# Kernel tuning notes

Hardware: AMD Instinct MI355X
Metric: run time of the kernel (lower is better)

The kernel has to match this reference:

```python
import jax, jax.numpy as jnp
import numpy as np

EMBED_DIM = 768
NUM_HEADS = 12
SEGMENT_LENGTHS = (2048, 4096, 8192)
DILATION_RATES = (1, 2, 4)
LN_EPS = 1e-5


def setup_inputs() -> dict:
    key = jax.random.key(0)
    ks = jax.random.split(key, 12)
    B, N, E = 2, 8192, EMBED_DIM
    xavier = (2.0 / (E + E)) ** 0.5  # xavier_normal_ std for square weight
    return {
        "query": jax.random.normal(ks[0], (B, N, E), jnp.float32),
        "key_": jax.random.normal(ks[1], (B, N, E), jnp.float32),
        "value": jax.random.normal(ks[2], (B, N, E), jnp.float32),
        "Wq": jax.random.normal(ks[3], (E, E), jnp.float32) * xavier,
        "bq": jnp.zeros((E,), jnp.float32),
        "Wk": jax.random.normal(ks[4], (E, E), jnp.float32) * xavier,
        "bk": jnp.zeros((E,), jnp.float32),
        "Wv": jax.random.normal(ks[5], (E, E), jnp.float32) * xavier,
        "bv": jnp.zeros((E,), jnp.float32),
        "Wo": jax.random.normal(ks[6], (E, E), jnp.float32) * xavier,
        "bo": jnp.zeros((E,), jnp.float32),
        "ln_g": jnp.ones((E,), jnp.float32),
        "ln_b": jnp.zeros((E,), jnp.float32),
    }


def _dilated_attention(q, k, v):
    # q,k,v: [b, n, h, d]  (LongNet dilated attention, non-causal)
    b, n, h, d = q.shape
    G = len(SEGMENT_LENGTHS)
    hpg = h // G  # heads per dilation group
    scale = 1.0 / jnp.sqrt(jnp.asarray(d, q.dtype))
    out = jnp.zeros_like(q)
    for i, (g, r) in enumerate(zip(SEGMENT_LENGTHS, DILATION_RATES)):
        offset = i % r
        hmin, hmax = i * hpg, (i + 1) * hpg
        def seg(x):
            # [b, n_seg, g, h, d] -> dilate within segment, slice head group
            xs = x.reshape(b, n // g, g, h, d)
            return xs[:, :, offset::r, hmin:hmax, :]  # [b, ns, s, hg, d]
        qs, ks_, vs = seg(q), seg(k), seg(v)
        # attention within each dilated segment
        scores = jnp.einsum("bnshd,bnthd->bnhst", qs, ks_) * scale
        attn = jax.nn.softmax(scores, axis=-1)
        xo = jnp.einsum("bnhst,bnthd->bnshd", attn, vs)
        out_r = out.reshape(b, n // g, g, h, d)
        out_r = out_r.at[:, :, offset::r, hmin:hmax, :].add(xo)
        out = out_r.reshape(b, n, h, d)
    return out / G


def reference(query, key_, value, Wq, bq, Wk, bk, Wv, bv, Wo, bo, ln_g, ln_b):
    b, n, e = query.shape
    h, d = NUM_HEADS, e // NUM_HEADS
    q = (query @ Wq.T + bq).reshape(b, n, h, d)
    k = (key_ @ Wk.T + bk).reshape(b, n, h, d)
    v = (value @ Wv.T + bv).reshape(b, n, h, d)
    x = _dilated_attention(q, k, v).reshape(b, n, e)
    mu = jnp.mean(x, axis=-1, keepdims=True)
    var = jnp.mean(jnp.square(x - mu), axis=-1, keepdims=True)
    x = (x - mu) * jax.lax.rsqrt(var + LN_EPS) * ln_g + ln_b
    return x @ Wo.T + bo
```

## Files before the change

kernel.cpp:

```cpp
#include <hip/hip_runtime.h>
#include <hip/hip_bf16.h>
#include <stdint.h>

typedef unsigned int uint32;
typedef unsigned short u16;
typedef __attribute__((ext_vector_type(4))) float f32x4;
typedef __attribute__((ext_vector_type(16))) float f32x16;
typedef __attribute__((ext_vector_type(8))) __bf16 bf16x8;
typedef __attribute__((ext_vector_type(8))) short i16x8;
typedef __attribute__((ext_vector_type(4))) short i16x4;
typedef __attribute__((ext_vector_type(4))) uint32 u32x4;

#define DEVINL static __device__ __forceinline__

DEVINL u16 f2bf(float f){
  uint32 u = __builtin_bit_cast(uint32, f);
  return (u16)((u + 0x7fffu + ((u >> 16) & 1u)) >> 16);
}

DEVINL uint32 cvtpk(float lo, float hi){
  uint32 r;
  asm("v_cvt_pk_bf16_f32 %0, %1, %2" : "=v"(r) : "v"(lo), "v"(hi));
  return r;
}

DEVINL void permswap(uint32 &a, uint32 &b){
  asm volatile("s_nop 1\n\tv_permlane32_swap_b32 %0, %1" : "+v"(a), "+v"(b));
}

DEVINL f32x4 mfma16(bf16x8 a, bf16x8 b, f32x4 c){
  return __builtin_amdgcn_mfma_f32_16x16x32_bf16(a, b, c, 0, 0, 0);
}
DEVINL f32x16 mfma32(bf16x8 a, bf16x8 b, f32x16 c){
  return __builtin_amdgcn_mfma_f32_32x32x16_bf16(a, b, c, 0, 0, 0);
}
DEVINL f32x16 zero16(){
  f32x16 z;
  #pragma unroll
  for (int r = 0; r < 16; ++r) z[r] = 0.f;
  return z;
}

DEVINL void gload16(const u16* g, u16* l){
  __builtin_amdgcn_global_load_lds(
      (const __attribute__((address_space(1))) uint32*)g,
      (__attribute__((address_space(3))) uint32*)l, 16, 0, 0);
}

static constexpr size_t ISTR = 2048 * 64;
static constexpr float QSCALE = 0.18033688011112042f;
static constexpr int LDA = 40;

__global__ void cvt_w4(const float* __restrict__ s0, const float* __restrict__ s1,
                       const float* __restrict__ s2, const float* __restrict__ s3,
                       u16* __restrict__ d0, u16* __restrict__ d1,
                       u16* __restrict__ d2, u16* __restrict__ d3, int n4){
  const int wsel = blockIdx.y;
  const float* src = wsel == 0 ? s0 : wsel == 1 ? s1 : wsel == 2 ? s2 : s3;
  u16* dst = wsel == 0 ? d0 : wsel == 1 ? d1 : wsel == 2 ? d2 : d3;
  int i = blockIdx.x * 256 + threadIdx.x;
  if (i < n4){
    f32x4 v = *(const f32x4*)(src + (size_t)i * 4);
    u16 o[4];
    #pragma unroll
    for (int j = 0; j < 4; ++j) o[j] = f2bf(v[j]);
    *(i16x4*)(dst + (size_t)i * 4) = *(const i16x4*)o;
  }
}

__global__ __launch_bounds__(256) void qkv_fused(
    const float* __restrict__ X0, const float* __restrict__ X1, const float* __restrict__ X2,
    const u16* __restrict__ W0, const u16* __restrict__ W1, const u16* __restrict__ W2,
    const float* __restrict__ b0, const float* __restrict__ b1, const float* __restrict__ b2,
    u16* __restrict__ Y0, u16* __restrict__ Y1, u16* __restrict__ Y2)
{
  __shared__ u16 As[2][128 * LDA];
  __shared__ u16 Bs[2][128 * 32];
  const int tid = threadIdx.x;
  const int l = tid & 63, w = tid >> 6;
  const int l15 = l & 15, lh = l >> 4;
  const int wr = w >> 1, wc = w & 1;
  const int yb = blockIdx.y;
  const int sect = yb / 6;
  const int row0 = blockIdx.x * 128, col0 = (yb % 6) * 128;

  const float* X   = sect == 0 ? X0 : sect == 1 ? X1 : X2;
  const u16*   W   = sect == 0 ? W0 : sect == 1 ? W1 : W2;
  const float* bia_p = sect == 0 ? b0 : sect == 1 ? b1 : b2;
  u16*         Yg  = sect == 0 ? Y0 : sect == 1 ? Y1 : Y2;
  const float scale = sect == 0 ? QSCALE : 1.0f;
  const int tmode = (sect == 2) ? 1 : 0;

  const int gr = l >> 2;
  const int gcx = ((l & 3) ^ ((gr >> 1) & 3)) * 8;
  const u16* wsrc0 = W + (size_t)(col0 + w * 32 + gr) * 768 + gcx;

  const int sr = tid >> 1, sc = (tid & 1) * 16;
  const float* asrc = X + (size_t)(row0 + sr) * 768 + sc;

  f32x4 acc[4][4];
  #pragma unroll
  for (int i = 0; i < 4; ++i)
    #pragma unroll
    for (int j = 0; j < 4; ++j) acc[i][j] = f32x4{0.f, 0.f, 0.f, 0.f};

  auto STAGE_B = [&](int buf, int ks){
    const u16* ws = wsrc0 + ks * 32;
    gload16(ws,            &Bs[buf][(w * 32) * 32]);
    gload16(ws + 16 * 768, &Bs[buf][(w * 32 + 16) * 32]);
  };
  auto WRITE_A = [&](int buf, f32x4 ra0, f32x4 ra1, f32x4 ra2, f32x4 ra3){
    u32x4 w0 = { cvtpk(ra0[0], ra0[1]), cvtpk(ra0[2], ra0[3]),
                 cvtpk(ra1[0], ra1[1]), cvtpk(ra1[2], ra1[3]) };
    u32x4 w1 = { cvtpk(ra2[0], ra2[1]), cvtpk(ra2[2], ra2[3]),
                 cvtpk(ra3[0], ra3[1]), cvtpk(ra3[2], ra3[3]) };
    *(i16x8*)&As[buf][sr * LDA + sc]     = __builtin_bit_cast(i16x8, w0);
    *(i16x8*)&As[buf][sr * LDA + sc + 8] = __builtin_bit_cast(i16x8, w1);
  };

  {
    STAGE_B(0, 0);
    f32x4 ra0 = *(const f32x4*)(asrc);
    f32x4 ra1 = *(const f32x4*)(asrc + 4);
    f32x4 ra2 = *(const f32x4*)(asrc + 8);
    f32x4 ra3 = *(const f32x4*)(asrc + 12);
    WRITE_A(0, ra0, ra1, ra2, ra3);
  }
  asm volatile("s_waitcnt vmcnt(0)");
  __syncthreads();

  const int bxor = ((l15 >> 1) & 3) * 8;
  int cur = 0;
  for (int ks = 0; ks < 24; ++ks) {
    const int nxt = cur ^ 1;
    f32x4 ra0, ra1, ra2, ra3;
    const bool has = ks < 23;
    if (has) {
      STAGE_B(nxt, ks + 1);
      const float* ap = asrc + (ks + 1) * 32;
      ra0 = *(const f32x4*)(ap);      ra1 = *(const f32x4*)(ap + 4);
      ra2 = *(const f32x4*)(ap + 8);  ra3 = *(const f32x4*)(ap + 12);
    }
    bf16x8 af[4], bfr[4];
    #pragma unroll
    for (int mi = 0; mi < 4; ++mi)
      af[mi] = *(const bf16x8*)&As[cur][(wr * 64 + mi * 16 + l15) * LDA + lh * 8];
    #pragma unroll
    for (int ni = 0; ni < 4; ++ni)
      bfr[ni] = *(const bf16x8*)&Bs[cur][(wc * 64 + ni * 16 + l15) * 32 + ((lh * 8) ^ bxor)];
    #pragma unroll
    for (int mi = 0; mi < 4; ++mi)
      #pragma unroll
      for (int ni = 0; ni < 4; ++ni)
        acc[mi][ni] = mfma16(af[mi], bfr[ni], acc[mi][ni]);
    if (has) WRITE_A(nxt, ra0, ra1, ra2, ra3);
    asm volatile("s_waitcnt vmcnt(0)");
    __syncthreads();
    cur = nxt;
  }

  #pragma unroll
  for (int ni = 0; ni < 4; ++ni) {
    const int e = col0 + wc * 64 + ni * 16 + l15;
    const int h = e >> 6, d = e & 63;
    const int grp = h >> 2, hg = h & 3;
    const int instB = (grp == 0) ? 0 : (grp == 1) ? 32 : 48;
    const float bia = bia_p[e];
    #pragma unroll
    for (int mi = 0; mi < 4; ++mi) {
      #pragma unroll
      for (int r = 0; r < 4; ++r) {
        const int row = row0 + wr * 64 + mi * 16 + lh * 4 + r;
        const int b = row >> 13, nn = row & 8191;
        const int p = nn & ((2048 << grp) - 1);
        if ((p & ((1 << grp) - 1)) != grp) continue;
        const int seg = nn >> (11 + grp);
        const int t = (p - grp) >> grp;
        const int inst = instB + ((b * (4 >> grp) + seg) << 2) + hg;
        const u16 val = f2bf((acc[mi][ni][r] + bia) * scale);
        if (tmode == 0) Yg[(size_t)inst * ISTR + (size_t)t * 64 + d] = val;
        else            Yg[(size_t)inst * ISTR + (size_t)d * 2048 + t] = val;
      }
    }
  }
}

__global__ __launch_bounds__(256) void dil_attn(
    const u16* __restrict__ Qg, const u16* __restrict__ Kg,
    const u16* __restrict__ VgT, uint32* __restrict__ Op32, float* __restrict__ Ls)
{
  __shared__ u16 Kb[2][64 * 64];
  __shared__ u16 Vb[2][64 * 64];
  const int tid = threadIdx.x;
  const int w = tid >> 6, l = tid & 63;
  const int l31 = l & 31, hi = l >> 5;
  const int id = blockIdx.x;
  const int nid = (id & 7) * 224 + (id >> 3);
  const int inst = nid >> 5, rem = nid & 31;
  const int qb = rem >> 1, kh = rem & 1;
  const size_t ibase = (size_t)inst * ISTR;
  const int qbase = qb * 128 + w * 32;
  const int k0base = kh * 1024;

  const u16* qlane = Qg + ibase + (size_t)(qbase + l31) * 64 + hi * 8;
  const bf16x8 qf0 = *(const bf16x8*)(qlane);
  const bf16x8 qf1 = *(const bf16x8*)(qlane + 16);
  const bf16x8 qf2 = *(const bf16x8*)(qlane + 32);
  const bf16x8 qf3 = *(const bf16x8*)(qlane + 48);

  const int srow = l >> 3;
  const int scol = ((l & 7) ^ (srow & 7)) << 3;
  const u16* kgs = Kg  + ibase + (size_t)srow * 64 + scol;
  const u16* vgs = VgT + ibase + (size_t)srow * 2048 + scol;

  f32x16 acc0 = zero16(), acc1 = zero16(), rs = zero16();
  const int sxor = (l31 & 7) << 3;
  const bf16x8 ones = __builtin_bit_cast(bf16x8,
      u32x4{0x3F803F80u, 0x3F803F80u, 0x3F803F80u, 0x3F803F80u});

  auto STAGE = [&](int buf, int k0){
    #pragma unroll
    for (int q = 0; q < 2; ++q){
      const int rb = w * 16 + q * 8;
      gload16(kgs + (size_t)(k0 + rb) * 64, &Kb[buf][rb * 64]);
      gload16(vgs + (size_t)rb * 2048 + k0, &Vb[buf][rb * 64]);
    }
  };

  STAGE(0, k0base);
  asm volatile("s_waitcnt vmcnt(0)");
  __syncthreads();

  int cur = 0;
  for (int step = 0; step < 16; ++step) {
    if (step < 15) STAGE(cur ^ 1, k0base + ((step + 1) << 6));
    const u16* kt = &Kb[cur][0];
    const u16* vt = &Vb[cur][0];
    #pragma unroll
    for (int s = 0; s < 2; ++s) {
      const int ksub = s * 32;
      const int krow = (ksub + l31) * 64;
      bf16x8 kc0 = *(const bf16x8*)&kt[krow + ((hi * 8)      ^ sxor)];
      bf16x8 kc1 = *(const bf16x8*)&kt[krow + ((16 + hi * 8) ^ sxor)];
      bf16x8 kc2 = *(const bf16x8*)&kt[krow + ((32 + hi * 8) ^ sxor)];
      bf16x8 kc3 = *(const bf16x8*)&kt[krow + ((48 + hi * 8) ^ sxor)];

      f32x16 sT = zero16();
      sT = mfma32(kc0, qf0, sT);
      sT = mfma32(kc1, qf1, sT);
      sT = mfma32(kc2, qf2, sT);
      sT = mfma32(kc3, qf3, sT);

      #pragma unroll
      for (int r = 0; r < 16; ++r) sT[r] = __builtin_amdgcn_exp2f(sT[r]);

      uint32 cw0 = cvtpk(sT[0],  sT[1]),  cw1 = cvtpk(sT[2],  sT[3]);
      uint32 cw2 = cvtpk(sT[4],  sT[5]),  cw3 = cvtpk(sT[6],  sT[7]);
      uint32 cw4 = cvtpk(sT[8],  sT[9]),  cw5 = cvtpk(sT[10], sT[11]);
      uint32 cw6 = cvtpk(sT[12], sT[13]), cw7 = cvtpk(sT[14], sT[15]);
      permswap(cw0, cw2); permswap(cw1, cw3);
      permswap(cw4, cw6); permswap(cw5, cw7);
      bf16x8 pa0 = __builtin_bit_cast(bf16x8, u32x4{cw0, cw1, cw2, cw3});
      bf16x8 pa1 = __builtin_bit_cast(bf16x8, u32x4{cw4, cw5, cw6, cw7});

      const int vr0 = l31 * 64, vr1 = (l31 + 32) * 64;
      bf16x8 v00 = *(const bf16x8*)&vt[vr0 + ((ksub + hi * 8)      ^ sxor)];
      bf16x8 v01 = *(const bf16x8*)&vt[vr0 + ((ksub + 16 + hi * 8) ^ sxor)];
      bf16x8 v10 = *(const bf16x8*)&vt[vr1 + ((ksub + hi * 8)      ^ sxor)];
      bf16x8 v11 = *(const bf16x8*)&vt[vr1 + ((ksub + 16 + hi * 8) ^ sxor)];

      rs   = mfma32(pa0, ones, rs);
      rs   = mfma32(pa1, ones, rs);
      acc0 = mfma32(pa0, v00, acc0);
      acc0 = mfma32(pa1, v01, acc0);
      acc1 = mfma32(pa0, v10, acc1);
      acc1 = mfma32(pa1, v11, acc1);
    }
    asm volatile("s_waitcnt vmcnt(0)");
    __syncthreads();
    cur ^= 1;
  }

  if (l31 == 0) {
    float* lsp = Ls + ((size_t)kh * 56 + inst) * 2048 + qbase;
    #pragma unroll
    for (int r = 0; r < 16; ++r) {
      const int qrow = (r & 3) + 8 * (r >> 2) + 4 * hi;
      lsp[qrow] = rs[r];
    }
  }
  uint32* op = Op32 + (size_t)kh * (56u * 2048u * 32u)
                    + ((size_t)inst * 2048 + qbase) * 32 + l31;
  #pragma unroll
  for (int r = 0; r < 16; ++r) {
    const int qrow = (r & 3) + 8 * (r >> 2) + 4 * hi;
    op[(size_t)qrow * 32] = cvtpk(acc0[r], acc1[r]);
  }
}

__global__ __launch_bounds__(256) void ln_gather(
    const uint32* __restrict__ Op32, const float* __restrict__ Ls,
    const float* __restrict__ gamma, const float* __restrict__ beta,
    u16* __restrict__ xln)
{
  const int row = blockIdx.x;
  const int b = row >> 13, nn = row & 8191;
  const int tid = threadIdx.x;
  const size_t KHOFF = 56u * 2048u * 32u;
  float v[3];
  #pragma unroll
  for (int j = 0; j < 3; ++j) {
    const int e = tid + j * 256;
    const int h = e >> 6, d = e & 63;
    const int grp = h >> 2, hg = h & 3;
    const int p = nn & ((2048 << grp) - 1);
    float val = 0.f;
    if ((p & ((1 << grp) - 1)) == grp) {
      const int seg = nn >> (11 + grp);
      const int instB = (grp == 0) ? 0 : (grp == 1) ? 32 : 48;
      const int inst = instB + ((b * (4 >> grp) + seg) << 2) + hg;
      const int t = (p - grp) >> grp;
      const size_t wbase = ((size_t)inst * 2048 + t) * 32 + (d & 31);
      const uint32 w0 = Op32[wbase];
      const uint32 w1 = Op32[wbase + KHOFF];
      const float o0 = __builtin_bit_cast(float, d < 32 ? (w0 << 16) : (w0 & 0xFFFF0000u));
      const float o1 = __builtin_bit_cast(float, d < 32 ? (w1 << 16) : (w1 & 0xFFFF0000u));
      const float s = Ls[(size_t)inst * 2048 + t] + Ls[(size_t)(56 * 2048) + inst * 2048 + t];
      val = (o0 + o1) * (1.0f / (3.0f * s));
    }
    v[j] = val;
  }
  float s = v[0] + v[1] + v[2];
  float q = v[0]*v[0] + v[1]*v[1] + v[2]*v[2];
  #pragma unroll
  for (int off = 1; off < 64; off <<= 1) { s += __shfl_xor(s, off); q += __shfl_xor(q, off); }
  __shared__ float red[8];
  const int w = tid >> 6, l = tid & 63;
  if (l == 0) { red[w] = s; red[4 + w] = q; }
  __syncthreads();
  s = red[0] + red[1] + red[2] + red[3];
  q = red[4] + red[5] + red[6] + red[7];
  const float mu = s * (1.f / 768.f);
  const float var = q * (1.f / 768.f) - mu * mu;
  const float rs = rsqrtf(var + 1e-5f);
  #pragma unroll
  for (int j = 0; j < 3; ++j) {
    const int e = tid + j * 256;
    xln[(size_t)row * 768 + e] = f2bf((v[j] - mu) * rs * gamma[e] + beta[e]);
  }
}

__global__ __launch_bounds__(256) void out_gemm(
    const u16* __restrict__ Xb, const u16* __restrict__ W,
    const float* __restrict__ bias, float* __restrict__ out)
{
  __shared__ u16 As[2][128 * 32];
  __shared__ u16 Bs[2][128 * 32];
  const int tid = threadIdx.x;
  const int l = tid & 63, w = tid >> 6;
  const int l15 = l & 15, lh = l >> 4;
  const int wr = w >> 1, wc = w & 1;
  const int row0 = blockIdx.x * 128, col0 = blockIdx.y * 128;

  const int gr = l >> 2;
  const int gcx = ((l & 3) ^ ((gr >> 1) & 3)) * 8;
  const u16* asrc0 = Xb + (size_t)(row0 + w * 32 + gr) * 768 + gcx;
  const u16* wsrc0 = W  + (size_t)(col0 + w * 32 + gr) * 768 + gcx;

  f32x4 acc[4][4];
  #pragma unroll
  for (int i = 0; i < 4; ++i)
    #pragma unroll
    for (int j = 0; j < 4; ++j) acc[i][j] = f32x4{0.f, 0.f, 0.f, 0.f};

  auto STAGE = [&](int buf, int ks){
    const u16* as = asrc0 + ks * 32;
    const u16* ws = wsrc0 + ks * 32;
    gload16(as,            &As[buf][(w * 32) * 32]);
    gload16(as + 16 * 768, &As[buf][(w * 32 + 16) * 32]);
    gload16(ws,            &Bs[buf][(w * 32) * 32]);
    gload16(ws + 16 * 768, &Bs[buf][(w * 32 + 16) * 32]);
  };

  STAGE(0, 0);
  asm volatile("s_waitcnt vmcnt(0)");
  __syncthreads();

  const int bxor = ((l15 >> 1) & 3) * 8;
  int cur = 0;
  for (int ks = 0; ks < 24; ++ks) {
    const int nxt = cur ^ 1;
    if (ks < 23) STAGE(nxt, ks + 1);
    bf16x8 af[4], bfr[4];
    #pragma unroll
    for (int mi = 0; mi < 4; ++mi)
      af[mi] = *(const bf16x8*)&As[cur][(wr * 64 + mi * 16 + l15) * 32 + ((lh * 8) ^ bxor)];
    #pragma unroll
    for (int ni = 0; ni < 4; ++ni)
      bfr[ni] = *(const bf16x8*)&Bs[cur][(wc * 64 + ni * 16 + l15) * 32 + ((lh * 8) ^ bxor)];
    #pragma unroll
    for (int mi = 0; mi < 4; ++mi)
      #pragma unroll
      for (int ni = 0; ni < 4; ++ni)
        acc[mi][ni] = mfma16(af[mi], bfr[ni], acc[mi][ni]);
    asm volatile("s_waitcnt vmcnt(0)");
    __syncthreads();
    cur = nxt;
  }

  #pragma unroll
  for (int ni = 0; ni < 4; ++ni) {
    const int e = col0 + wc * 64 + ni * 16 + l15;
    const float bia = bias[e];
    #pragma unroll
    for (int mi = 0; mi < 4; ++mi) {
      #pragma unroll
      for (int r = 0; r < 4; ++r) {
        const int row = row0 + wr * 64 + mi * 16 + lh * 4 + r;
        out[(size_t)row * 768 + e] = acc[mi][ni][r] + bia;
      }
    }
  }
}

extern "C" void kernel_launch(void* const* d_in, const int* in_sizes, int n_in,
                              void* d_out, int out_size, void* d_ws, size_t ws_size,
                              hipStream_t stream) {
  const float* query = (const float*)d_in[0];
  const float* key_  = (const float*)d_in[1];
  const float* value = (const float*)d_in[2];
  const float* Wq = (const float*)d_in[3];
  const float* bq = (const float*)d_in[4];
  const float* Wk = (const float*)d_in[5];
  const float* bk = (const float*)d_in[6];
  const float* Wv = (const float*)d_in[7];
  const float* bv = (const float*)d_in[8];
  const float* Wo = (const float*)d_in[9];
  const float* bo = (const float*)d_in[10];
  const float* lng = (const float*)d_in[11];
  const float* lnb = (const float*)d_in[12];

  char* ws = (char*)d_ws;
  size_t off = 0;
  auto alloc = [&](size_t bytes) { size_t o = off; off += (bytes + 255) & ~(size_t)255; return o; };
  const size_t WB = 768 * 768 * 2;
  const size_t GB = (size_t)56 * ISTR * 2;
  u16* wqb = (u16*)(ws + alloc(WB));
  u16* wkb = (u16*)(ws + alloc(WB));
  u16* wvb = (u16*)(ws + alloc(WB));
  u16* wob = (u16*)(ws + alloc(WB));
  u16* Qg  = (u16*)(ws + alloc(GB));
  u16* Kg  = (u16*)(ws + alloc(GB));
  u16* VgT = (u16*)(ws + alloc(GB));
  uint32* Op32 = (uint32*)(ws + alloc((size_t)2 * 56 * 2048 * 32 * 4));
  float* Lsb  = (float*)(ws + alloc((size_t)2 * 56 * 2048 * 4));
  u16* xln = (u16*)(ws + alloc((size_t)16384 * 768 * 2));

  const int n4 = 768 * 768 / 4;
  cvt_w4<<<dim3(576, 4), 256, 0, stream>>>(Wq, Wk, Wv, Wo, wqb, wkb, wvb, wob, n4);

  qkv_fused<<<dim3(128, 18), 256, 0, stream>>>(
      query, key_, value, wqb, wkb, wvb, bq, bk, bv, Qg, Kg, VgT);

  dil_attn<<<dim3(1792), 256, 0, stream>>>(Qg, Kg, VgT, Op32, Lsb);
  ln_gather<<<dim3(16384), 256, 0, stream>>>(Op32, Lsb, lng, lnb, xln);
  out_gemm<<<dim3(128, 6), 256, 0, stream>>>(xln, wob, bo, (float*)d_out);
}
```

Measured before the change: 287.3 us.

## Triple-buffer GEMM k-loops with async LDS loads; convert fp32 A in compute

Both the QKV projection and the output GEMM move from a double-buffered loop to a three-stage ring with prefetch distance two. The loop now waits on a partial vmcnt, so one tile's loads stay in flight during compute. In the QKV kernel, the fp32 activation tile is no longer staged through registers and converted before the LDS store. It is copied straight to LDS with global_load_lds in an XOR-swizzled layout and converted to bf16 at fragment-read time. This removes register staging and exposed global latency, but costs more LDS (an fp32 A tile times three buffers), which may lower occupancy, and repeats the conversion work in every wave.

```diff
diff --git a/kernel.cpp b/kernel.cpp
--- a/kernel.cpp
+++ b/kernel.cpp
@@ -46,10 +46,14 @@
       (const __attribute__((address_space(1))) uint32*)g,
       (__attribute__((address_space(3))) uint32*)l, 16, 0, 0);
 }
+DEVINL void gload16f(const float* g, float* l){
+  __builtin_amdgcn_global_load_lds(
+      (const __attribute__((address_space(1))) uint32*)g,
+      (__attribute__((address_space(3))) uint32*)l, 16, 0, 0);
+}
 
 static constexpr size_t ISTR = 2048 * 64;
 static constexpr float QSCALE = 0.18033688011112042f;
-static constexpr int LDA = 40;
 
 __global__ void cvt_w4(const float* __restrict__ s0, const float* __restrict__ s1,
                        const float* __restrict__ s2, const float* __restrict__ s3,
@@ -74,8 +78,8 @@
     const float* __restrict__ b0, const float* __restrict__ b1, const float* __restrict__ b2,
     u16* __restrict__ Y0, u16* __restrict__ Y1, u16* __restrict__ Y2)
 {
-  __shared__ u16 As[2][128 * LDA];
-  __shared__ u16 Bs[2][128 * 32];
+  __shared__ float Af[3][128 * 32];
+  __shared__ u16  Bs[3][128 * 32];
   const int tid = threadIdx.x;
   const int l = tid & 63, w = tid >> 6;
   const int l15 = l & 15, lh = l >> 4;
@@ -95,8 +99,9 @@
   const int gcx = ((l & 3) ^ ((gr >> 1) & 3)) * 8;
   const u16* wsrc0 = W + (size_t)(col0 + w * 32 + gr) * 768 + gcx;
 
-  const int sr = tid >> 1, sc = (tid & 1) * 16;
-  const float* asrc = X + (size_t)(row0 + sr) * 768 + sc;
+  const int ar = l >> 3;
+  const int acx = ((l & 7) ^ (ar & 7)) * 4;
+  const float* asrc0 = X + (size_t)(row0 + w * 32 + ar) * 768 + acx;
 
   f32x4 acc[4][4];
   #pragma unroll
@@ -104,60 +109,56 @@
     #pragma unroll
     for (int j = 0; j < 4; ++j) acc[i][j] = f32x4{0.f, 0.f, 0.f, 0.f};
 
-  auto STAGE_B = [&](int buf, int ks){
-    const u16* ws = wsrc0 + ks * 32;
-    gload16(ws,            &Bs[buf][(w * 32) * 32]);
-    gload16(ws + 16 * 768, &Bs[buf][(w * 32 + 16) * 32]);
+  auto STAGE = [&](int buf, int ks){
+    const u16* wsp = wsrc0 + ks * 32;
+    gload16(wsp,            &Bs[buf][(w * 32) * 32]);
+    gload16(wsp + 16 * 768, &Bs[buf][(w * 32 + 16) * 32]);
+    const float* asp = asrc0 + ks * 32;
+    gload16f(asp,            &Af[buf][(w * 32) * 32]);
+    gload16f(asp +  8 * 768, &Af[buf][(w * 32 +  8) * 32]);
+    gload16f(asp + 16 * 768, &Af[buf][(w * 32 + 16) * 32]);
+    gload16f(asp + 24 * 768, &Af[buf][(w * 32 + 24) * 32]);
   };
-  auto WRITE_A = [&](int buf, f32x4 ra0, f32x4 ra1, f32x4 ra2, f32x4 ra3){
-    u32x4 w0 = { cvtpk(ra0[0], ra0[1]), cvtpk(ra0[2], ra0[3]),
-                 cvtpk(ra1[0], ra1[1]), cvtpk(ra1[2], ra1[3]) };
-    u32x4 w1 = { cvtpk(ra2[0], ra2[1]), cvtpk(ra2[2], ra2[3]),
-                 cvtpk(ra3[0], ra3[1]), cvtpk(ra3[2], ra3[3]) };
-    *(i16x8*)&As[buf][sr * LDA + sc]     = __builtin_bit_cast(i16x8, w0);
-    *(i16x8*)&As[buf][sr * LDA + sc + 8] = __builtin_bit_cast(i16x8, w1);
-  };
-
-  {
-    STAGE_B(0, 0);
-    f32x4 ra0 = *(const f32x4*)(asrc);
-    f32x4 ra1 = *(const f32x4*)(asrc + 4);
-    f32x4 ra2 = *(const f32x4*)(asrc + 8);
-    f32x4 ra3 = *(const f32x4*)(asrc + 12);
-    WRITE_A(0, ra0, ra1, ra2, ra3);
-  }
-  asm volatile("s_waitcnt vmcnt(0)");
-  __syncthreads();
 
   const int bxor = ((l15 >> 1) & 3) * 8;
-  int cur = 0;
-  for (int ks = 0; ks < 24; ++ks) {
-    const int nxt = cur ^ 1;
-    f32x4 ra0, ra1, ra2, ra3;
-    const bool has = ks < 23;
-    if (has) {
-      STAGE_B(nxt, ks + 1);
-      const float* ap = asrc + (ks + 1) * 32;
-      ra0 = *(const f32x4*)(ap);      ra1 = *(const f32x4*)(ap + 4);
-      ra2 = *(const f32x4*)(ap + 8);  ra3 = *(const f32x4*)(ap + 12);
-    }
+  const int rx = l15 & 7;
+
+  auto COMPUTE = [&](int buf){
     bf16x8 af[4], bfr[4];
     #pragma unroll
-    for (int mi = 0; mi < 4; ++mi)
-      af[mi] = *(const bf16x8*)&As[cur][(wr * 64 + mi * 16 + l15) * LDA + lh * 8];
+    for (int mi = 0; mi < 4; ++mi) {
+      const int r = wr * 64 + mi * 16 + l15;
+      const int c0 = (lh * 2) ^ rx, c1 = (lh * 2 + 1) ^ rx;
+      f32x4 p0 = *(const f32x4*)&Af[buf][r * 32 + c0 * 4];
+      f32x4 p1 = *(const f32x4*)&Af[buf][r * 32 + c1 * 4];
+      u32x4 pk = { cvtpk(p0[0], p0[1]), cvtpk(p0[2], p0[3]),
+                   cvtpk(p1[0], p1[1]), cvtpk(p1[2], p1[3]) };
+      af[mi] = __builtin_bit_cast(bf16x8, pk);
+    }
     #pragma unroll
     for (int ni = 0; ni < 4; ++ni)
-      bfr[ni] = *(const bf16x8*)&Bs[cur][(wc * 64 + ni * 16 + l15) * 32 + ((lh * 8) ^ bxor)];
+      bfr[ni] = *(const bf16x8*)&Bs[buf][(wc * 64 + ni * 16 + l15) * 32 + ((lh * 8) ^ bxor)];
     #pragma unroll
     for (int mi = 0; mi < 4; ++mi)
       #pragma unroll
       for (int ni = 0; ni < 4; ++ni)
         acc[mi][ni] = mfma16(af[mi], bfr[ni], acc[mi][ni]);
-    if (has) WRITE_A(nxt, ra0, ra1, ra2, ra3);
-    asm volatile("s_waitcnt vmcnt(0)");
+  };
+
+  STAGE(0, 0);
+  STAGE(1, 1);
+  int cur = 0, stg = 2;
+  for (int ks = 0; ks < 23; ++ks) {
+    asm volatile("s_waitcnt vmcnt(6)" ::: "memory");
     __syncthreads();
-    cur = nxt;
-  }
+    if (ks < 22) STAGE(stg, ks + 2);
+    COMPUTE(cur);
+    cur = (cur == 2) ? 0 : cur + 1;
+    stg = (stg == 2) ? 0 : stg + 1;
+  }
+  asm volatile("s_waitcnt vmcnt(0)" ::: "memory");
+  __syncthreads();
+  COMPUTE(cur);
 
   #pragma unroll
   for (int ni = 0; ni < 4; ++ni) {
@@ -354,8 +355,8 @@
     const u16* __restrict__ Xb, const u16* __restrict__ W,
     const float* __restrict__ bias, float* __restrict__ out)
 {
-  __shared__ u16 As[2][128 * 32];
-  __shared__ u16 Bs[2][128 * 32];
+  __shared__ u16 As[3][128 * 32];
+  __shared__ u16 Bs[3][128 * 32];
   const int tid = threadIdx.x;
   const int l = tid & 63, w = tid >> 6;
   const int l15 = l & 15, lh = l >> 4;
@@ -382,31 +383,36 @@
     gload16(ws + 16 * 768, &Bs[buf][(w * 32 + 16) * 32]);
   };
 
-  STAGE(0, 0);
-  asm volatile("s_waitcnt vmcnt(0)");
-  __syncthreads();
-
   const int bxor = ((l15 >> 1) & 3) * 8;
-  int cur = 0;
-  for (int ks = 0; ks < 24; ++ks) {
-    const int nxt = cur ^ 1;
-    if (ks < 23) STAGE(nxt, ks + 1);
+  auto COMPUTE = [&](int buf){
     bf16x8 af[4], bfr[4];
     #pragma unroll
     for (int mi = 0; mi < 4; ++mi)
-      af[mi] = *(const bf16x8*)&As[cur][(wr * 64 + mi * 16 + l15) * 32 + ((lh * 8) ^ bxor)];
+      af[mi] = *(const bf16x8*)&As[buf][(wr * 64 + mi * 16 + l15) * 32 + ((lh * 8) ^ bxor)];
     #pragma unroll
     for (int ni = 0; ni < 4; ++ni)
-      bfr[ni] = *(const bf16x8*)&Bs[cur][(wc * 64 + ni * 16 + l15) * 32 + ((lh * 8) ^ bxor)];
+      bfr[ni] = *(const bf16x8*)&Bs[buf][(wc * 64 + ni * 16 + l15) * 32 + ((lh * 8) ^ bxor)];
     #pragma unroll
     for (int mi = 0; mi < 4; ++mi)
       #pragma unroll
       for (int ni = 0; ni < 4; ++ni)
         acc[mi][ni] = mfma16(af[mi], bfr[ni], acc[mi][ni]);
-    asm volatile("s_waitcnt vmcnt(0)");
+  };
+
+  STAGE(0, 0);
+  STAGE(1, 1);
+  int cur = 0, stg = 2;
+  for (int ks = 0; ks < 23; ++ks) {
+    asm volatile("s_waitcnt vmcnt(4)" ::: "memory");
     __syncthreads();
-    cur = nxt;
-  }
+    if (ks < 22) STAGE(stg, ks + 2);
+    COMPUTE(cur);
+    cur = (cur == 2) ? 0 : cur + 1;
+    stg = (stg == 2) ? 0 : stg + 1;
+  }
+  asm volatile("s_waitcnt vmcnt(0)" ::: "memory");
+  __syncthreads();
+  COMPUTE(cur);
 
   #pragma unroll
   for (int ni = 0; ni < 4; ++ni) {
```

Measured after the change: 317.7 us. 10.6% more time.

## Pre-convert activations to bf16 and stage A via direct global-to-LDS loads

Applied to the files above, without the earlier changes.

Adds a separate kernel that converts query/key/value from fp32 to bf16 into a workspace region, which is then aliased with the later attention buffers. The QKV GEMM now loads the A tile straight into LDS with global_load_lds using the same swizzle as B, replacing per-tile fp32 register loads, conversion and LDS stores. The aim is a simpler GEMM pipeline that moves half as many A bytes. The cost is an extra pass that reads 150MB of fp32 and writes 75MB of bf16, plus one more kernel launch. The weight converter also switches to the packed convert instruction.

```diff
diff --git a/kernel.cpp b/kernel.cpp
--- a/kernel.cpp
+++ b/kernel.cpp
@@ -9,6 +9,7 @@
 typedef __attribute__((ext_vector_type(8))) __bf16 bf16x8;
 typedef __attribute__((ext_vector_type(8))) short i16x8;
 typedef __attribute__((ext_vector_type(4))) short i16x4;
+typedef __attribute__((ext_vector_type(2))) uint32 u32x2;
 typedef __attribute__((ext_vector_type(4))) uint32 u32x4;
 
 #define DEVINL static __device__ __forceinline__
@@ -49,7 +50,6 @@
 
 static constexpr size_t ISTR = 2048 * 64;
 static constexpr float QSCALE = 0.18033688011112042f;
-static constexpr int LDA = 40;
 
 __global__ void cvt_w4(const float* __restrict__ s0, const float* __restrict__ s1,
                        const float* __restrict__ s2, const float* __restrict__ s3,
@@ -61,20 +61,32 @@
   int i = blockIdx.x * 256 + threadIdx.x;
   if (i < n4){
     f32x4 v = *(const f32x4*)(src + (size_t)i * 4);
-    u16 o[4];
-    #pragma unroll
-    for (int j = 0; j < 4; ++j) o[j] = f2bf(v[j]);
-    *(i16x4*)(dst + (size_t)i * 4) = *(const i16x4*)o;
+    u32x2 o = { cvtpk(v[0], v[1]), cvtpk(v[2], v[3]) };
+    *(u32x2*)(dst + (size_t)i * 4) = o;
+  }
+}
+
+__global__ void cvt_x(const float* __restrict__ s0, const float* __restrict__ s1,
+                      const float* __restrict__ s2,
+                      u16* __restrict__ d0, u16* __restrict__ d1, u16* __restrict__ d2){
+  const int t = blockIdx.y;
+  const float* src = t == 0 ? s0 : t == 1 ? s1 : s2;
+  u16* dst = t == 0 ? d0 : t == 1 ? d1 : d2;
+  const int n4 = 16384 * 768 / 4;
+  for (int i = blockIdx.x * 256 + threadIdx.x; i < n4; i += gridDim.x * 256){
+    f32x4 v = *(const f32x4*)(src + (size_t)i * 4);
+    u32x2 o = { cvtpk(v[0], v[1]), cvtpk(v[2], v[3]) };
+    *(u32x2*)(dst + (size_t)i * 4) = o;
   }
 }
 
 __global__ __launch_bounds__(256) void qkv_fused(
-    const float* __restrict__ X0, const float* __restrict__ X1, const float* __restrict__ X2,
+    const u16* __restrict__ X0, const u16* __restrict__ X1, const u16* __restrict__ X2,
     const u16* __restrict__ W0, const u16* __restrict__ W1, const u16* __restrict__ W2,
     const float* __restrict__ b0, const float* __restrict__ b1, const float* __restrict__ b2,
     u16* __restrict__ Y0, u16* __restrict__ Y1, u16* __restrict__ Y2)
 {
-  __shared__ u16 As[2][128 * LDA];
+  __shared__ u16 As[2][128 * 32];
   __shared__ u16 Bs[2][128 * 32];
   const int tid = threadIdx.x;
   const int l = tid & 63, w = tid >> 6;
@@ -84,48 +96,34 @@
   const int sect = yb / 6;
   const int row0 = blockIdx.x * 128, col0 = (yb % 6) * 128;
 
-  const float* X   = sect == 0 ? X0 : sect == 1 ? X1 : X2;
-  const u16*   W   = sect == 0 ? W0 : sect == 1 ? W1 : W2;
+  const u16* X = sect == 0 ? X0 : sect == 1 ? X1 : X2;
+  const u16* W = sect == 0 ? W0 : sect == 1 ? W1 : W2;
   const float* bia_p = sect == 0 ? b0 : sect == 1 ? b1 : b2;
-  u16*         Yg  = sect == 0 ? Y0 : sect == 1 ? Y1 : Y2;
+  u16* Yg = sect == 0 ? Y0 : sect == 1 ? Y1 : Y2;
   const float scale = sect == 0 ? QSCALE : 1.0f;
   const int tmode = (sect == 2) ? 1 : 0;
 
   const int gr = l >> 2;
   const int gcx = ((l & 3) ^ ((gr >> 1) & 3)) * 8;
+  const u16* asrc0 = X + (size_t)(row0 + w * 32 + gr) * 768 + gcx;
   const u16* wsrc0 = W + (size_t)(col0 + w * 32 + gr) * 768 + gcx;
 
-  const int sr = tid >> 1, sc = (tid & 1) * 16;
-  const float* asrc = X + (size_t)(row0 + sr) * 768 + sc;
-
   f32x4 acc[4][4];
   #pragma unroll
   for (int i = 0; i < 4; ++i)
     #pragma unroll
     for (int j = 0; j < 4; ++j) acc[i][j] = f32x4{0.f, 0.f, 0.f, 0.f};
 
-  auto STAGE_B = [&](int buf, int ks){
+  auto STAGE = [&](int buf, int ks){
+    const u16* as = asrc0 + ks * 32;
     const u16* ws = wsrc0 + ks * 32;
+    gload16(as,            &As[buf][(w * 32) * 32]);
+    gload16(as + 16 * 768, &As[buf][(w * 32 + 16) * 32]);
     gload16(ws,            &Bs[buf][(w * 32) * 32]);
     gload16(ws + 16 * 768, &Bs[buf][(w * 32 + 16) * 32]);
   };
-  auto WRITE_A = [&](int buf, f32x4 ra0, f32x4 ra1, f32x4 ra2, f32x4 ra3){
-    u32x4 w0 = { cvtpk(ra0[0], ra0[1]), cvtpk(ra0[2], ra0[3]),
-                 cvtpk(ra1[0], ra1[1]), cvtpk(ra1[2], ra1[3]) };
-    u32x4 w1 = { cvtpk(ra2[0], ra2[1]), cvtpk(ra2[2], ra2[3]),
-                 cvtpk(ra3[0], ra3[1]), cvtpk(ra3[2], ra3[3]) };
-    *(i16x8*)&As[buf][sr * LDA + sc]     = __builtin_bit_cast(i16x8, w0);
-    *(i16x8*)&As[buf][sr * LDA + sc + 8] = __builtin_bit_cast(i16x8, w1);
-  };
-
-  {
-    STAGE_B(0, 0);
-    f32x4 ra0 = *(const f32x4*)(asrc);
-    f32x4 ra1 = *(const f32x4*)(asrc + 4);
-    f32x4 ra2 = *(const f32x4*)(asrc + 8);
-    f32x4 ra3 = *(const f32x4*)(asrc + 12);
-    WRITE_A(0, ra0, ra1, ra2, ra3);
-  }
+
+  STAGE(0, 0);
   asm volatile("s_waitcnt vmcnt(0)");
   __syncthreads();
 
@@ -133,18 +131,11 @@
   int cur = 0;
   for (int ks = 0; ks < 24; ++ks) {
     const int nxt = cur ^ 1;
-    f32x4 ra0, ra1, ra2, ra3;
-    const bool has = ks < 23;
-    if (has) {
-      STAGE_B(nxt, ks + 1);
-      const float* ap = asrc + (ks + 1) * 32;
-      ra0 = *(const f32x4*)(ap);      ra1 = *(const f32x4*)(ap + 4);
-      ra2 = *(const f32x4*)(ap + 8);  ra3 = *(const f32x4*)(ap + 12);
-    }
+    if (ks < 23) STAGE(nxt, ks + 1);
     bf16x8 af[4], bfr[4];
     #pragma unroll
     for (int mi = 0; mi < 4; ++mi)
-      af[mi] = *(const bf16x8*)&As[cur][(wr * 64 + mi * 16 + l15) * LDA + lh * 8];
+      af[mi] = *(const bf16x8*)&As[cur][(wr * 64 + mi * 16 + l15) * 32 + ((lh * 8) ^ bxor)];
     #pragma unroll
     for (int ni = 0; ni < 4; ++ni)
       bfr[ni] = *(const bf16x8*)&Bs[cur][(wc * 64 + ni * 16 + l15) * 32 + ((lh * 8) ^ bxor)];
@@ -153,7 +144,6 @@
       #pragma unroll
       for (int ni = 0; ni < 4; ++ni)
         acc[mi][ni] = mfma16(af[mi], bfr[ni], acc[mi][ni]);
-    if (has) WRITE_A(nxt, ra0, ra1, ra2, ra3);
     asm volatile("s_waitcnt vmcnt(0)");
     __syncthreads();
     cur = nxt;
@@ -445,6 +435,10 @@
   auto alloc = [&](size_t bytes) { size_t o = off; off += (bytes + 255) & ~(size_t)255; return o; };
   const size_t WB = 768 * 768 * 2;
   const size_t GB = (size_t)56 * ISTR * 2;
+  const size_t XB = (size_t)16384 * 768 * 2;
+  const size_t OPB = (size_t)2 * 56 * 2048 * 32 * 4;
+  const size_t LSB = (size_t)2 * 56 * 2048 * 4;
+
   u16* wqb = (u16*)(ws + alloc(WB));
   u16* wkb = (u16*)(ws + alloc(WB));
   u16* wvb = (u16*)(ws + alloc(WB));
@@ -452,15 +446,22 @@
   u16* Qg  = (u16*)(ws + alloc(GB));
   u16* Kg  = (u16*)(ws + alloc(GB));
   u16* VgT = (u16*)(ws + alloc(GB));
-  uint32* Op32 = (uint32*)(ws + alloc((size_t)2 * 56 * 2048 * 32 * 4));
-  float* Lsb  = (float*)(ws + alloc((size_t)2 * 56 * 2048 * 4));
-  u16* xln = (u16*)(ws + alloc((size_t)16384 * 768 * 2));
+
+  const size_t regionSz = ((3 * XB > OPB + LSB + 256 * 2 + XB) ? 3 * XB : OPB + LSB + 256 * 2 + XB) + 1024;
+  char* region = ws + alloc(regionSz);
+  u16* Xq = (u16*)(region);
+  u16* Xk = (u16*)(region + XB);
+  u16* Xv = (u16*)(region + 2 * XB);
+  uint32* Op32 = (uint32*)(region);
+  float*  Lsb  = (float*)(region + ((OPB + 255) & ~(size_t)255));
+  u16*    xln  = (u16*)(region + ((OPB + 255) & ~(size_t)255) + ((LSB + 255) & ~(size_t)255));
 
   const int n4 = 768 * 768 / 4;
   cvt_w4<<<dim3(576, 4), 256, 0, stream>>>(Wq, Wk, Wv, Wo, wqb, wkb, wvb, wob, n4);
+  cvt_x<<<dim3(1536, 3), 256, 0, stream>>>(query, key_, value, Xq, Xk, Xv);
 
   qkv_fused<<<dim3(128, 18), 256, 0, stream>>>(
-      query, key_, value, wqb, wkb, wvb, bq, bk, bv, Qg, Kg, VgT);
+      Xq, Xk, Xv, wqb, wkb, wvb, bq, bk, bv, Qg, Kg, VgT);
 
   dil_attn<<<dim3(1792), 256, 0, stream>>>(Qg, Kg, VgT, Op32, Lsb);
   ln_gather<<<dim3(16384), 256, 0, stream>>>(Op32, Lsb, lng, lnb, xln);
```

Result: faster. 279.0 us (median of 2 runs) (-2.9%).
